# Kernel tuning notes

Measured on AMD Instinct MI355X. Metric: run time of the kernel, lower is better.

The kernel has to match this reference:

```python
import jax, jax.numpy as jnp
import numpy as np

B, TQ, TK, D, NA = 8, 512, 2048, 1024, 512
H, HD = 16, 64          # n_head, head_dim (D = H*HD)
NE, HID = 4, 32         # n_experts, expert hidden_dim
EPS = 1e-6


def _rmsnorm(x, w):
    return x * jax.lax.rsqrt(jnp.mean(x * x, axis=-1, keepdims=True) + EPS) * w


def setup_inputs() -> dict:
    key = jax.random.key(0)
    ks = jax.random.split(key, 20)
    r = lambda i, shp: jax.random.normal(ks[i], shp, dtype=jnp.float32) * 0.02
    return {
        'q': jax.random.normal(ks[0], (B, TQ, D), dtype=jnp.float32),
        'kv': jax.random.normal(ks[1], (B, TK, D), dtype=jnp.float32),
        'qn_w': jnp.ones((D,), jnp.float32),
        'kva_w': jnp.ones((D,), jnp.float32),
        'kvi_w': jnp.ones((D,), jnp.float32),
        'dn_w': jnp.ones((D,), jnp.float32),
        'fn_w': jnp.ones((D,), jnp.float32),
        'Wq': r(2, (D, D)), 'bq': jnp.zeros((D,), jnp.float32),
        'Wk': r(3, (D, D)), 'bk': jnp.zeros((D,), jnp.float32),
        'Wv': r(4, (D, D)), 'bv': jnp.zeros((D,), jnp.float32),
        'Wo': r(5, (D, D)), 'bo': jnp.zeros((D,), jnp.float32),
        'active_bias': r(6, (D,)),
        'inactive_bias': r(7, (D,)),
        'log_temp': jnp.array(0.0, jnp.float32),
        'gate_attn': jnp.array(0.3, jnp.float32),
        'gate_ffn': jnp.array(0.7, jnp.float32),
        'Wr': r(8, (D, NE)), 'br': jnp.zeros((NE,), jnp.float32),
        'W1': r(9, (NE, D, 2 * HID)), 'b1': jnp.zeros((NE, 2 * HID), jnp.float32),
        'W2': r(10, (NE, HID, D)), 'b2': jnp.zeros((NE, D), jnp.float32),
        'kv_mask': jnp.ones((B, TK), bool),
        'n_actives': NA,
    }


def _forward(q, kv, qn_w, kva_w, kvi_w, dn_w, fn_w,
             Wq, bq, Wk, bk, Wv, bv, Wo, bo,
             active_bias, inactive_bias, log_temp, gate_attn, gate_ffn,
             Wr, br, W1, b1, W2, b2, kv_mask, n_actives):
    Na = int(n_actives)
    Tk = kv.shape[1]
    Ni = Tk - Na
    b, tq, d = q.shape

    # split-normed kv, with active/inactive learned biases injected pre-KV-proj
    kv_a = _rmsnorm(kv[:, :Na], kva_w) + active_bias
    kv_i = _rmsnorm(kv[:, Na:], kvi_w) + inactive_bias
    kv_b = jnp.concatenate([kv_a, kv_i], axis=1)

    qn = _rmsnorm(q, qn_w)
    qp = (qn @ Wq + bq).reshape(b, tq, H, HD).transpose(0, 2, 1, 3)  # (B,H,Tq,hd)
    k = (kv_b @ Wk + bk).reshape(b, Tk, H, HD).transpose(0, 2, 1, 3)
    v = (kv_b @ Wv + bv).reshape(b, Tk, H, HD).transpose(0, 2, 1, 3)

    # torch: q *= 1/sqrt(hd), then SDPA(q/temp, ...) applies another 1/sqrt(hd)
    temp = jnp.clip(jnp.exp(log_temp), 0.1, 10.0)
    scale = 1.0 / (HD * temp)

    def attn(kk, vv):
        logits = jnp.einsum('bhqd,bhkd->bhqk', qp, kk) * scale
        return jnp.einsum('bhqk,bhkd->bhqd', jax.nn.softmax(logits, axis=-1), vv)

    out = attn(k[:, :, :Na], v[:, :, :Na]) / np.sqrt(max(Na, 1)) \
        - attn(k[:, :, Na:], v[:, :, Na:]) / np.sqrt(max(Ni, 1))
    out = out.transpose(0, 2, 1, 3).reshape(b, tq, d)
    delta = _rmsnorm(out @ Wo + bo, dn_w)
    q_new = q + jax.nn.sigmoid(gate_attn) * delta

    # dense soft MoE over normed kv, with query-similarity logit bias
    x = _rmsnorm(kv, fn_w)
    logits = x @ Wr + br                                   # (B,Tk,NE)
    q_vec = jnp.mean(q_new, axis=1, keepdims=True)         # (B,1,D)
    sim = jnp.einsum('bqd,btd->bt', q_vec, x)              # (B,Tk)
    probs = jax.nn.softmax(logits + sim[..., None], axis=-1)

    h = jnp.einsum('btd,edh->bteh', x, W1) + b1            # (B,Tk,NE,2*HID)
    xp, g = h[..., :HID], h[..., HID:]
    act = xp * (g * jax.nn.sigmoid(g))                     # SwiGLU
    eo = jnp.einsum('bteh,ehd->bted', act, W2) + b2        # (B,Tk,NE,D)
    moe_out = jnp.einsum('bte,bted->btd', probs, eo)

    kv_new = kv + jax.nn.sigmoid(gate_ffn) * moe_out
    return q_new, kv_new


def reference(q, kv, qn_w, kva_w, kvi_w, dn_w, fn_w,
              Wq, bq, Wk, bk, Wv, bv, Wo, bo,
              active_bias, inactive_bias, log_temp, gate_attn, gate_ffn,
              Wr, br, W1, b1, W2, b2, kv_mask, n_actives):
    return _forward(q, kv, qn_w, kva_w, kvi_w, dn_w, fn_w,
                    Wq, bq, Wk, bk, Wv, bv, Wo, bo,
                    active_bias, inactive_bias, log_temp, gate_attn, gate_ffn,
                    Wr, br, W1, b1, W2, b2, kv_mask, n_actives)
```

## Files before the change

### kernel.cpp

```cpp
#include <hip/hip_runtime.h>
#include <hip/hip_bf16.h>
#include <stdint.h>


#define B_   8
#define TQ_  512
#define TK_  2048
#define D_   1024
#define H_   16
#define HD_  64
#define NE_  4
#define HID_ 32
#define EPSF 1e-6f
#define LOG2E 1.44269504f

typedef __bf16 bf16_t;
typedef __bf16 bf16x8 __attribute__((ext_vector_type(8)));
typedef __bf16 bf16x4 __attribute__((ext_vector_type(4)));
typedef float  f32x4  __attribute__((ext_vector_type(4)));

typedef __attribute__((address_space(1))) void gvoid_t;
typedef __attribute__((address_space(3))) void lvoid_t;

__device__ __forceinline__ void gld_lds16(const void* g, void* l) {
  __builtin_amdgcn_global_load_lds((gvoid_t*)g, (lvoid_t*)l, 16, 0, 0);
}

struct TP4 { const float* in[4]; bf16_t* out[4]; };

__global__ void transpose_conv4_kernel(TP4 p) {
  __shared__ float tile[32][33];
  const int bz = blockIdx.z;
  const float* in = p.in[bz];
  bf16_t* out = p.out[bz];
  const int rb = blockIdx.y * 32, cb = blockIdx.x * 32;
  const int txi = threadIdx.x, tyi = threadIdx.y;
#pragma unroll
  for (int i = 0; i < 32; i += 8)
    tile[tyi + i][txi] = in[(size_t)(rb + tyi + i) * D_ + cb + txi];
  __syncthreads();
#pragma unroll
  for (int i = 0; i < 32; i += 8)
    out[(size_t)(cb + tyi + i) * D_ + rb + txi] = (bf16_t)tile[txi][tyi + i];
}

__global__ void transpose_conv_kernel(const float* __restrict__ in, bf16_t* __restrict__ out,
                                      int R, int C, int in_bstride,
                                      int out_rstride, int ob_row, int ob_col) {
  __shared__ float tile[32][33];
  const int bz = blockIdx.z;
  const int rb = blockIdx.y * 32, cb = blockIdx.x * 32;
  const int txi = threadIdx.x, tyi = threadIdx.y;
  const float* inp = in + (size_t)bz * in_bstride;
#pragma unroll
  for (int i = 0; i < 32; i += 8) {
    const int r = rb + tyi + i, c = cb + txi;
    if (r < R && c < C) tile[tyi + i][txi] = inp[(size_t)r * C + c];
  }
  __syncthreads();
#pragma unroll
  for (int i = 0; i < 32; i += 8) {
    const int orow = cb + tyi + i;
    const int ocol = rb + txi;
    if (orow < C && ocol < R)
      out[(size_t)(orow + bz * ob_row) * out_rstride + bz * ob_col + ocol] =
          (bf16_t)tile[txi][tyi + i];
  }
}

__device__ __forceinline__ float block_rsum(float v, float* red) {
  v += __shfl_xor(v, 1);  v += __shfl_xor(v, 2);  v += __shfl_xor(v, 4);
  v += __shfl_xor(v, 8);  v += __shfl_xor(v, 16); v += __shfl_xor(v, 32);
  const int tid = threadIdx.x;
  if ((tid & 63) == 0) red[tid >> 6] = v;
  __syncthreads();
  return red[0] + red[1] + red[2] + red[3];
}

__global__ __launch_bounds__(256)
void rms_kv_kernel(const float* __restrict__ kv, const float* __restrict__ kva_w,
                   const float* __restrict__ kvi_w, const float* __restrict__ fn_w,
                   const float* __restrict__ ab, const float* __restrict__ ib,
                   const int* __restrict__ n_act, const float* __restrict__ Wr,
                   const float* __restrict__ br,
                   bf16_t* __restrict__ kvb, bf16_t* __restrict__ xn,
                   float* __restrict__ probs) {
  __shared__ float red[4];
  __shared__ f32x4 pred[4];
  const int row = blockIdx.x;
  const int t = row & (TK_ - 1);
  const int tid = threadIdx.x;
  const float* src = kv + (size_t)row * D_;
  f32x4 v = ((const f32x4*)src)[tid];
  float ss = v[0]*v[0] + v[1]*v[1] + v[2]*v[2] + v[3]*v[3];
  ss = block_rsum(ss, red);
  const float rs = rsqrtf(ss * (1.0f / D_) + EPSF);
  const int Na = n_act[0];
  const float* wsel = (t < Na) ? kva_w : kvi_w;
  const float* bsel = (t < Na) ? ab : ib;
  const int d = tid * 4;
  f32x4 wv = *(const f32x4*)(wsel + d);
  f32x4 bv = *(const f32x4*)(bsel + d);
  f32x4 fv = *(const f32x4*)(fn_w + d);
  bf16x4 o0, o1;
  f32x4 p4 = {};
#pragma unroll
  for (int c = 0; c < 4; ++c) {
    const float xv = v[c] * rs;
    const float xf = xv * fv[c];
    o0[c] = (bf16_t)(xv * wv[c] + bv[c]);
    o1[c] = (bf16_t)xf;
    const f32x4 w4 = *(const f32x4*)&Wr[(d + c) * 4];
    p4 += w4 * xf;
  }
  *(bf16x4*)&kvb[(size_t)row * D_ + d] = o0;
  *(bf16x4*)&xn [(size_t)row * D_ + d] = o1;
#pragma unroll
  for (int m = 1; m <= 32; m <<= 1) {
    p4[0] += __shfl_xor(p4[0], m); p4[1] += __shfl_xor(p4[1], m);
    p4[2] += __shfl_xor(p4[2], m); p4[3] += __shfl_xor(p4[3], m);
  }
  if ((tid & 63) == 0) pred[tid >> 6] = p4;
  __syncthreads();
  if (tid == 0) {
    f32x4 s = pred[0] + pred[1] + pred[2] + pred[3];
    s[0] += br[0]; s[1] += br[1]; s[2] += br[2]; s[3] += br[3];
    const float mx = fmaxf(fmaxf(s[0], s[1]), fmaxf(s[2], s[3]));
    const float e0 = __expf(s[0] - mx), e1 = __expf(s[1] - mx);
    const float e2 = __expf(s[2] - mx), e3 = __expf(s[3] - mx);
    const float inv = 1.0f / (e0 + e1 + e2 + e3);
    f32x4 pr = { e0 * inv, e1 * inv, e2 * inv, e3 * inv };
    *(f32x4*)&probs[row * 4] = pr;
  }
}

__global__ __launch_bounds__(256)
void rms_q_kernel(const float* __restrict__ q, const float* __restrict__ qn_w,
                  bf16_t* __restrict__ qn) {
  __shared__ float red[4];
  const int row = blockIdx.x;
  const int tid = threadIdx.x;
  const float* src = q + (size_t)row * D_;
  f32x4 v = ((const f32x4*)src)[tid];
  float ss = v[0]*v[0] + v[1]*v[1] + v[2]*v[2] + v[3]*v[3];
  ss = block_rsum(ss, red);
  const float rs = rsqrtf(ss * (1.0f / D_) + EPSF);
  const int d = tid * 4;
  f32x4 wv = *(const f32x4*)(qn_w + d);
  bf16x4 o0;
#pragma unroll
  for (int c = 0; c < 4; ++c) o0[c] = (bf16_t)(v[c] * rs * wv[c]);
  *(bf16x4*)&qn[(size_t)row * D_ + d] = o0;
}

__device__ __forceinline__ int xcd_swz(int bx, int gx) {
  if ((gx & 7) == 0) { const int cpx = gx >> 3; return (bx & 7) * cpx + (bx >> 3); }
  return bx;
}

__global__ __launch_bounds__(256)
void gemm_kv(const bf16_t* __restrict__ A, const bf16_t* __restrict__ Wk,
             const bf16_t* __restrict__ Wv, const float* __restrict__ bk,
             const float* __restrict__ bv, bf16_t* __restrict__ Kout,
             bf16_t* __restrict__ Vt) {
  __shared__ alignas(16) bf16_t lds[3 * 8192];
  bf16_t* As  = lds;
  bf16_t* Bks = lds + 8192;
  bf16_t* Bvs = lds + 16384;
  const int K = D_;
  const int tid = threadIdx.x;
  const int lane = tid & 63;
  const int w = tid >> 6;
  const int wr = w >> 1, wc = w & 1;
  const int lane15 = lane & 15, lgrp = lane >> 4;

  const int flat = blockIdx.x;
  const int xcd = flat & 7;
  const int local = flat >> 3;
  const int tg = local >> 3;
  const int yy = local & 7;
  const int m0 = (xcd * 16 + tg) * 128;
  const int n0 = yy * 128;

  f32x4 acc_k[4][4] = {};
  f32x4 acc_v[4][4] = {};

  const bf16_t* ga = A  + (size_t)(m0 + (tid >> 2)) * K + (tid & 3) * 8;
  const bf16_t* gk = Wk + (size_t)(n0 + (tid >> 2)) * K + (tid & 3) * 8;
  const bf16_t* gv = Wv + (size_t)(n0 + (tid >> 2)) * K + (tid & 3) * 8;
  const size_t rstep = (size_t)64 * K;
  const int kb = lgrp * 8;
  const int ar  = ((wr * 64 + lane15) << 5) + kb;
  const int br2 = ((wc * 64 + lane15) << 5) + kb;

  gld_lds16(ga,         &As[tid * 8]);
  gld_lds16(ga + rstep, &As[2048 + tid * 8]);
  gld_lds16(gk,         &Bks[tid * 8]);
  gld_lds16(gk + rstep, &Bks[2048 + tid * 8]);
  gld_lds16(gv,         &Bvs[tid * 8]);
  gld_lds16(gv + rstep, &Bvs[2048 + tid * 8]);
  int buf = 0;
  for (int k0 = 0; k0 < K; k0 += 32) {
    __syncthreads();
    if (k0 + 32 < K) {
      const int nb = buf ^ 1;
      gld_lds16(ga + k0 + 32,         &As[nb * 4096 + tid * 8]);
      gld_lds16(ga + k0 + 32 + rstep, &As[nb * 4096 + 2048 + tid * 8]);
      gld_lds16(gk + k0 + 32,         &Bks[nb * 4096 + tid * 8]);
      gld_lds16(gk + k0 + 32 + rstep, &Bks[nb * 4096 + 2048 + tid * 8]);
      gld_lds16(gv + k0 + 32,         &Bvs[nb * 4096 + tid * 8]);
      gld_lds16(gv + k0 + 32 + rstep, &Bvs[nb * 4096 + 2048 + tid * 8]);
    }
    bf16x8 af[4], bkf[4], bvf[4];
#pragma unroll
    for (int i = 0; i < 4; ++i) af[i]  = *(const bf16x8*)&As [buf * 4096 + ar  + i * 512];
#pragma unroll
    for (int j = 0; j < 4; ++j) bkf[j] = *(const bf16x8*)&Bks[buf * 4096 + br2 + j * 512];
#pragma unroll
    for (int j = 0; j < 4; ++j) bvf[j] = *(const bf16x8*)&Bvs[buf * 4096 + br2 + j * 512];
    __builtin_amdgcn_s_setprio(1);
#pragma unroll
    for (int i = 0; i < 4; ++i)
#pragma unroll
      for (int j = 0; j < 4; ++j) {
        acc_k[i][j] = __builtin_amdgcn_mfma_f32_16x16x32_bf16(af[i], bkf[j], acc_k[i][j], 0, 0, 0);
        acc_v[i][j] = __builtin_amdgcn_mfma_f32_16x16x32_bf16(af[i], bvf[j], acc_v[i][j], 0, 0, 0);
      }
    __builtin_amdgcn_s_setprio(0);
    buf ^= 1;
  }

  const int row0 = m0 + wr * 64 + (lgrp << 2);
  const int col0 = n0 + wc * 64 + lane15;
#pragma unroll
  for (int j = 0; j < 4; ++j) {
    const int cc = col0 + j * 16;
    const float bkv = bk[cc];
#pragma unroll
    for (int i = 0; i < 4; ++i) {
      const int rr = row0 + i * 16;
#pragma unroll
      for (int r = 0; r < 4; ++r)
        Kout[(size_t)(rr + r) * D_ + cc] = (bf16_t)(acc_k[i][j][r] + bkv);
    }
  }

  __syncthreads();
  bf16_t* vt_l = lds + w * 4608;
#pragma unroll
  for (int j = 0; j < 4; ++j) {
    const int nl = j * 16 + lane15;
    const float bvv = bv[n0 + wc * 64 + nl];
#pragma unroll
    for (int i = 0; i < 4; ++i) {
      bf16x4 pv;
#pragma unroll
      for (int r = 0; r < 4; ++r) pv[r] = (bf16_t)(acc_v[i][j][r] + bvv);
      *(bf16x4*)&vt_l[nl * 72 + i * 16 + lgrp * 4] = pv;
    }
  }
  const int bidx2 = m0 >> 11;
  const int tok0 = (m0 & (TK_ - 1)) + wr * 64;
  bf16_t* vbase = Vt + (size_t)bidx2 * D_ * TK_ + (size_t)(n0 + wc * 64) * TK_ + tok0;
#pragma unroll
  for (int it = 0; it < 8; ++it) {
    const int ln = (lane >> 3) + it * 8;
    const int tk = (lane & 7) * 8;
    const bf16x8 v8 = *(const bf16x8*)&vt_l[ln * 72 + tk];
    *(bf16x8*)&vbase[(size_t)ln * TK_ + tk] = v8;
  }
}

__device__ __forceinline__ void gemm_loop_db(const bf16_t* __restrict__ ga,
                                             const bf16_t* __restrict__ gb,
                                             bf16_t* As, bf16_t* Bs, int K,
                                             size_t rstep, int ar, int br2,
                                             int tid, f32x4 acc[4][4]) {
  gld_lds16(ga,         &As[tid * 8]);
  gld_lds16(ga + rstep, &As[2048 + tid * 8]);
  gld_lds16(gb,         &Bs[tid * 8]);
  gld_lds16(gb + rstep, &Bs[2048 + tid * 8]);
  int buf = 0;
  for (int k0 = 0; k0 < K; k0 += 32) {
    __syncthreads();
    if (k0 + 32 < K) {
      const int nb = buf ^ 1;
      gld_lds16(ga + k0 + 32,         &As[nb * 4096 + tid * 8]);
      gld_lds16(ga + k0 + 32 + rstep, &As[nb * 4096 + 2048 + tid * 8]);
      gld_lds16(gb + k0 + 32,         &Bs[nb * 4096 + tid * 8]);
      gld_lds16(gb + k0 + 32 + rstep, &Bs[nb * 4096 + 2048 + tid * 8]);
    }
    bf16x8 af[4], bfr[4];
#pragma unroll
    for (int i = 0; i < 4; ++i) af[i]  = *(const bf16x8*)&As[buf * 4096 + ar  + i * 512];
#pragma unroll
    for (int j = 0; j < 4; ++j) bfr[j] = *(const bf16x8*)&Bs[buf * 4096 + br2 + j * 512];
#pragma unroll
    for (int i = 0; i < 4; ++i)
#pragma unroll
      for (int j = 0; j < 4; ++j)
        acc[i][j] = __builtin_amdgcn_mfma_f32_16x16x32_bf16(af[i], bfr[j], acc[i][j], 0, 0, 0);
    buf ^= 1;
  }
}

__device__ __forceinline__ void gemm64_loop_db(const bf16_t* __restrict__ ga,
                                               const bf16_t* __restrict__ gb,
                                               bf16_t* As, bf16_t* Bs, int K,
                                               size_t rstep, int ar, int br2,
                                               int tid, f32x4 acc[2][4]) {
  gld_lds16(ga,         &As[tid * 8]);
  gld_lds16(gb,         &Bs[tid * 8]);
  gld_lds16(gb + rstep, &Bs[2048 + tid * 8]);
  int buf = 0;
  for (int k0 = 0; k0 < K; k0 += 32) {
    __syncthreads();
    if (k0 + 32 < K) {
      const int nb = buf ^ 1;
      gld_lds16(ga + k0 + 32,         &As[nb * 2048 + tid * 8]);
      gld_lds16(gb + k0 + 32,         &Bs[nb * 4096 + tid * 8]);
      gld_lds16(gb + k0 + 32 + rstep, &Bs[nb * 4096 + 2048 + tid * 8]);
    }
    bf16x8 af[2], bfr[4];
#pragma unroll
    for (int i = 0; i < 2; ++i) af[i]  = *(const bf16x8*)&As[buf * 2048 + ar  + i * 512];
#pragma unroll
    for (int j = 0; j < 4; ++j) bfr[j] = *(const bf16x8*)&Bs[buf * 4096 + br2 + j * 512];
#pragma unroll
    for (int i = 0; i < 2; ++i)
#pragma unroll
      for (int j = 0; j < 4; ++j)
        acc[i][j] = __builtin_amdgcn_mfma_f32_16x16x32_bf16(af[i], bfr[j], acc[i][j], 0, 0, 0);
    buf ^= 1;
  }
}

template<int HAS_BIAS>
__global__ __launch_bounds__(256)
void gemm64_tn(const bf16_t* __restrict__ A, const bf16_t* __restrict__ Wt,
               const float* __restrict__ bias, bf16_t* __restrict__ C,
               int M, int N, int K) {
  __shared__ alignas(16) bf16_t As[2 * 64 * 32];
  __shared__ alignas(16) bf16_t Bs[2 * 128 * 32];
  const int tid = threadIdx.x;
  const int lane = tid & 63;
  const int w = tid >> 6;
  const int wr = w >> 1, wc = w & 1;
  const int m0 = xcd_swz(blockIdx.x, gridDim.x) * 64;
  const int n0 = blockIdx.y * 128;

  f32x4 acc[2][4] = {};
  const bf16_t* ga = A  + (size_t)(m0 + (tid >> 2)) * K + (tid & 3) * 8;
  const bf16_t* gb = Wt + (size_t)(n0 + (tid >> 2)) * K + (tid & 3) * 8;
  const int kb = (lane >> 4) * 8;
  const int ar  = ((wr * 32 + (lane & 15)) << 5) + kb;
  const int br2 = ((wc * 64 + (lane & 15)) << 5) + kb;

  gemm64_loop_db(ga, gb, As, Bs, K, (size_t)64 * K, ar, br2, tid, acc);

  const int row0 = m0 + wr * 32 + ((lane >> 4) << 2);
  const int col0 = n0 + wc * 64 + (lane & 15);
#pragma unroll
  for (int j = 0; j < 4; ++j) {
    const int cc = col0 + j * 16;
    const float bv = HAS_BIAS ? bias[cc] : 0.0f;
#pragma unroll
    for (int i = 0; i < 2; ++i) {
      const int rr = row0 + i * 16;
#pragma unroll
      for (int r = 0; r < 4; ++r)
        C[(size_t)(rr + r) * N + cc] = (bf16_t)(acc[i][j][r] + bv);
    }
  }
}

__global__ __launch_bounds__(256)
void gemm64_h_act(const bf16_t* __restrict__ A, const bf16_t* __restrict__ Wt,
                  const float* __restrict__ bias, const float* __restrict__ probs,
                  bf16_t* __restrict__ a2) {
  __shared__ alignas(16) bf16_t As[2 * 64 * 32];
  __shared__ alignas(16) bf16_t Bs[2 * 128 * 32];
  const int K = D_;
  const int tid = threadIdx.x;
  const int lane = tid & 63;
  const int w = tid >> 6;
  const int wr = w >> 1, wc = w & 1;
  const int m0 = xcd_swz(blockIdx.x, gridDim.x) * 64;
  const int n0 = blockIdx.y * 128;

  f32x4 acc[2][4] = {};
  const bf16_t* ga = A  + (size_t)(m0 + (tid >> 2)) * K + (tid & 3) * 8;
  const bf16_t* gb = Wt + (size_t)(n0 + (tid >> 2)) * K + (tid & 3) * 8;
  const int kb = (lane >> 4) * 8;
  const int ar  = ((wr * 32 + (lane & 15)) << 5) + kb;
  const int br2 = ((wc * 64 + (lane & 15)) << 5) + kb;

  gemm64_loop_db(ga, gb, As, Bs, K, (size_t)64 * K, ar, br2, tid, acc);

  const int row0 = m0 + wr * 32 + ((lane >> 4) << 2);
  const int hbase = n0 + wc * 64 + (lane & 15);
  const int e = hbase >> 6;
#pragma unroll
  for (int j = 0; j < 2; ++j) {
    const int ch = hbase + j * 16;
    const float bx = bias[ch], bg = bias[ch + 32];
    const int ac = (ch & 63) + e * 32;
#pragma unroll
    for (int i = 0; i < 2; ++i) {
      const int rr = row0 + i * 16;
#pragma unroll
      for (int r = 0; r < 4; ++r) {
        const float xp = acc[i][j][r] + bx;
        const float g  = acc[i][j + 2][r] + bg;
        const float sg = 1.0f / (1.0f + __expf(-g));
        const float pr = probs[(size_t)(rr + r) * 4 + e];
        a2[(size_t)(rr + r) * 128 + ac] = (bf16_t)(pr * xp * g * sg);
      }
    }
  }
}

__global__ __launch_bounds__(256)
void gemm_moe_kvnew(const bf16_t* __restrict__ A, const bf16_t* __restrict__ Wt,
                    const float* __restrict__ kv, const float* __restrict__ probs,
                    const float* __restrict__ b2, const float* __restrict__ gate_ffn,
                    float* __restrict__ out) {
  __shared__ alignas(16) bf16_t As[2 * 128 * 32];
  __shared__ alignas(16) bf16_t Bs[2 * 128 * 32];
  const int K = 128, N = D_;
  const int tid = threadIdx.x;
  const int lane = tid & 63;
  const int w = tid >> 6;
  const int wr = w >> 1, wc = w & 1;
  const int m0 = xcd_swz(blockIdx.x, gridDim.x) * 128;
  const int n0 = blockIdx.y * 128;

  f32x4 acc[4][4] = {};
  const bf16_t* ga = A  + (size_t)(m0 + (tid >> 2)) * K + (tid & 3) * 8;
  const bf16_t* gb = Wt + (size_t)(n0 + (tid >> 2)) * K + (tid & 3) * 8;
  const int kb = (lane >> 4) * 8;
  const int ar  = ((wr * 64 + (lane & 15)) << 5) + kb;
  const int br2 = ((wc * 64 + (lane & 15)) << 5) + kb;

  gemm_loop_db(ga, gb, As, Bs, K, (size_t)64 * K, ar, br2, tid, acc);

  const float sgf = 1.0f / (1.0f + __expf(-gate_ffn[0]));
  const int row0 = m0 + wr * 64 + ((lane >> 4) << 2);
  const int col0 = n0 + wc * 64 + (lane & 15);
#pragma unroll
  for (int j = 0; j < 4; ++j) {
    const int cc = col0 + j * 16;
    const f32x4 b2v = { b2[0 * D_ + cc], b2[1 * D_ + cc], b2[2 * D_ + cc], b2[3 * D_ + cc] };
#pragma unroll
    for (int i = 0; i < 4; ++i) {
      const int rr = row0 + i * 16;
#pragma unroll
      for (int r = 0; r < 4; ++r) {
        const f32x4 pr = *(const f32x4*)&probs[(size_t)(rr + r) * 4];
        const float bsum = pr[0]*b2v[0] + pr[1]*b2v[1] + pr[2]*b2v[2] + pr[3]*b2v[3];
        out[(size_t)(rr + r) * N + cc] =
            kv[(size_t)(rr + r) * N + cc] + sgf * (acc[i][j][r] + bsum);
      }
    }
  }
}

__global__ __launch_bounds__(128, 2)
void attn_mfma_kernel(const bf16_t* __restrict__ qp, const bf16_t* __restrict__ kb,
                      const bf16_t* __restrict__ vt, bf16_t* __restrict__ attno,
                      const float* __restrict__ log_temp, const int* __restrict__ n_act) {
  __shared__ alignas(16) bf16_t Ks[2][64 * 64];
  __shared__ alignas(16) bf16_t Vs[2][64 * 64];
  __shared__ alignas(16) bf16_t Ps[2][32 * 64];

  const int dd = blockIdx.x;
  const int xcd = dd & 7, within = dd >> 3;
  const int qt = within & 7, slot0 = within >> 3;
  const int bh = slot0 * 8 + xcd;
  const int b = bh >> 4, h = bh & 15;

  const int tid = threadIdx.x;
  const int lane = tid & 63;
  const int w = tid >> 6;
  const int lane15 = lane & 15, lgrp = lane >> 4, l7 = lane & 7;
  const int Na = n_act[0];
  float temp = __expf(log_temp[0]);
  temp = fminf(fmaxf(temp, 0.1f), 10.0f);
  const float lsc = LOG2E / (64.0f * temp);
  const int rowbase = qt * 64 + w * 32;

  const bf16_t* qsrcA = qp + (size_t)(b * TQ_ + rowbase + lane15) * D_ + h * 64 + lgrp * 8;
  const bf16_t* qsrcB = qsrcA + (size_t)16 * D_;
  bf16x8 qfA0 = *(const bf16x8*)qsrcA;
  bf16x8 qfA1 = *(const bf16x8*)(qsrcA + 32);
  bf16x8 qfB0 = *(const bf16x8*)qsrcB;
  bf16x8 qfB1 = *(const bf16x8*)(qsrcB + 32);
#pragma unroll
  for (int j = 0; j < 8; ++j) {
    qfA0[j] = (bf16_t)((float)qfA0[j] * lsc);
    qfA1[j] = (bf16_t)((float)qfA1[j] * lsc);
    qfB0[j] = (bf16_t)((float)qfB0[j] * lsc);
    qfB1[j] = (bf16_t)((float)qfB1[j] * lsc);
  }

  const int srow = tid >> 3;
  const int schunk = (tid & 7) ^ (srow & 7);
  const bf16_t* ksrc = kb + (size_t)(b * TK_ + srow) * D_ + h * 64 + schunk * 8;
  const bf16_t* vsrc = vt + ((size_t)(b * 16 + h) * 64 + srow) * TK_ + schunk * 8;

  f32x4 oA[4] = {}, oB[4] = {}, outA[4] = {}, outB[4] = {};
  float laccA = 0.f, laccB = 0.f;

  const float inv_sa = rsqrtf((float)(Na > 1 ? Na : 1));
  const int Ni = TK_ - Na;
  const float inv_si = rsqrtf((float)(Ni > 1 ? Ni : 1));

#pragma unroll
  for (int r = 0; r < 4; ++r) {
    gld_lds16(ksrc + (size_t)r * 16 * D_, &Ks[0][r * 1024 + tid * 8]);
    gld_lds16(vsrc + (size_t)r * 16 * TK_, &Vs[0][r * 1024 + tid * 8]);
  }

  for (int t = 0; t < TK_ / 64; ++t) {
    const int cur = t & 1;
    __syncthreads();
    if (t + 1 < TK_ / 64) {
      const int nb = cur ^ 1;
      const bf16_t* kN = ksrc + (size_t)(t + 1) * 64 * D_;
      const bf16_t* vN = vsrc + (size_t)(t + 1) * 64;
#pragma unroll
      for (int r = 0; r < 4; ++r) {
        gld_lds16(kN + (size_t)r * 16 * D_, &Ks[nb][r * 1024 + tid * 8]);
        gld_lds16(vN + (size_t)r * 16 * TK_, &Vs[nb][r * 1024 + tid * 8]);
      }
    }

    f32x4 sA[4], sB[4];
    __builtin_amdgcn_s_setprio(1);
#pragma unroll
    for (int cf = 0; cf < 4; ++cf) {
      const int krow = (cf * 16 + lane15) * 64;
      const bf16x8 kf0 = *(const bf16x8*)&Ks[cur][krow + ((lgrp ^ l7) << 3)];
      const bf16x8 kf1 = *(const bf16x8*)&Ks[cur][krow + (((lgrp + 4) ^ l7) << 3)];
      f32x4 s = {};
      s = __builtin_amdgcn_mfma_f32_16x16x32_bf16(kf0, qfA0, s, 0, 0, 0);
      s = __builtin_amdgcn_mfma_f32_16x16x32_bf16(kf1, qfA1, s, 0, 0, 0);
      sA[cf] = s;
      f32x4 s2 = {};
      s2 = __builtin_amdgcn_mfma_f32_16x16x32_bf16(kf0, qfB0, s2, 0, 0, 0);
      s2 = __builtin_amdgcn_mfma_f32_16x16x32_bf16(kf1, qfB1, s2, 0, 0, 0);
      sB[cf] = s2;
    }
    __builtin_amdgcn_s_setprio(0);

#pragma unroll
    for (int cf = 0; cf < 4; ++cf) {
      const int c = cf * 2 + (lgrp >> 1);
      const int pcol = ((c ^ l7) << 3) + (lgrp & 1) * 4;
      f32x4 pA, pB;
#pragma unroll
      for (int r = 0; r < 4; ++r) pA[r] = exp2f(sA[cf][r]);
#pragma unroll
      for (int r = 0; r < 4; ++r) pB[r] = exp2f(sB[cf][r]);
      laccA += (pA[0] + pA[1]) + (pA[2] + pA[3]);
      laccB += (pB[0] + pB[1]) + (pB[2] + pB[3]);
      bf16x4 pvA, pvB;
#pragma unroll
      for (int r = 0; r < 4; ++r) { pvA[r] = (bf16_t)pA[r]; pvB[r] = (bf16_t)pB[r]; }
      *(bf16x4*)&Ps[w][lane15 * 64 + pcol]        = pvA;
      *(bf16x4*)&Ps[w][(16 + lane15) * 64 + pcol] = pvB;
    }

    {
      const int prowA = lane15 * 64;
      const int prowB = (16 + lane15) * 64;
      const bf16x8 paA0 = *(const bf16x8*)&Ps[w][prowA + ((lgrp ^ l7) << 3)];
      const bf16x8 paA1 = *(const bf16x8*)&Ps[w][prowA + (((lgrp + 4) ^ l7) << 3)];
      const bf16x8 paB0 = *(const bf16x8*)&Ps[w][prowB + ((lgrp ^ l7) << 3)];
      const bf16x8 paB1 = *(const bf16x8*)&Ps[w][prowB + (((lgrp + 4) ^ l7) << 3)];
      __builtin_amdgcn_s_setprio(1);
#pragma unroll
      for (int df = 0; df < 4; ++df) {
        const int vrow = (df * 16 + lane15) * 64;
        const bf16x8 vf0 = *(const bf16x8*)&Vs[cur][vrow + ((lgrp ^ l7) << 3)];
        const bf16x8 vf1 = *(const bf16x8*)&Vs[cur][vrow + (((lgrp + 4) ^ l7) << 3)];
        oA[df] = __builtin_amdgcn_mfma_f32_16x16x32_bf16(paA0, vf0, oA[df], 0, 0, 0);
        oA[df] = __builtin_amdgcn_mfma_f32_16x16x32_bf16(paA1, vf1, oA[df], 0, 0, 0);
        oB[df] = __builtin_amdgcn_mfma_f32_16x16x32_bf16(paB0, vf0, oB[df], 0, 0, 0);
        oB[df] = __builtin_amdgcn_mfma_f32_16x16x32_bf16(paB1, vf1, oB[df], 0, 0, 0);
      }
      __builtin_amdgcn_s_setprio(0);
    }

    const bool endA = ((t + 1) * 64 == Na);
    const bool endI = (t == TK_ / 64 - 1);
    if (endA || endI) {
      float lA = laccA, lB = laccB;
      lA += __shfl_xor(lA, 16); lA += __shfl_xor(lA, 32);
      lB += __shfl_xor(lB, 16); lB += __shfl_xor(lB, 32);
      const float ssc = endA ? inv_sa : -inv_si;
      f32x4 ivA, ivB;
#pragma unroll
      for (int r = 0; r < 4; ++r) {
        ivA[r] = ssc / __shfl(lA, lgrp * 4 + r);
        ivB[r] = ssc / __shfl(lB, lgrp * 4 + r);
      }
#pragma unroll
      for (int df = 0; df < 4; ++df) {
        outA[df] += oA[df] * ivA; oA[df] = (f32x4){};
        outB[df] += oB[df] * ivB; oB[df] = (f32x4){};
      }
      laccA = 0.f; laccB = 0.f;
    }
  }

#pragma unroll
  for (int df = 0; df < 4; ++df)
#pragma unroll
    for (int r = 0; r < 4; ++r) {
      const size_t ro = (size_t)(b * TQ_ + rowbase + lgrp * 4 + r) * D_ + h * 64 + df * 16 + lane15;
      attno[ro]           = (bf16_t)outA[df][r];
      attno[ro + 16 * D_] = (bf16_t)outB[df][r];
    }
}

__global__ __launch_bounds__(256)
void delta_qnew_kernel(const bf16_t* __restrict__ proj, const float* __restrict__ dn_w,
                       const float* __restrict__ q, const float* __restrict__ gate_attn,
                       float* __restrict__ qnew) {
  __shared__ float red[4];
  const int row = blockIdx.x;
  const int tid = threadIdx.x;
  bf16x4 pv = *(const bf16x4*)(proj + (size_t)row * D_ + tid * 4);
  f32x4 v;
#pragma unroll
  for (int c = 0; c < 4; ++c) v[c] = (float)pv[c];
  float ss = v[0]*v[0] + v[1]*v[1] + v[2]*v[2] + v[3]*v[3];
  ss = block_rsum(ss, red);
  const float rs = rsqrtf(ss * (1.0f / D_) + EPSF);
  const float sga = 1.0f / (1.0f + __expf(-gate_attn[0]));
  const int d = tid * 4;
  f32x4 wv = *(const f32x4*)(dn_w + d);
  f32x4 qv = *(const f32x4*)(q + (size_t)row * D_ + d);
  f32x4 out;
#pragma unroll
  for (int c = 0; c < 4; ++c) out[c] = qv[c] + sga * (v[c] * rs * wv[c]);
  *(f32x4*)&qnew[(size_t)row * D_ + d] = out;
}

extern "C" void kernel_launch(void* const* d_in, const int* in_sizes, int n_in,
                              void* d_out, int out_size, void* d_ws, size_t ws_size,
                              hipStream_t stream) {
  const float* q           = (const float*)d_in[0];
  const float* kv          = (const float*)d_in[1];
  const float* qn_w        = (const float*)d_in[2];
  const float* kva_w       = (const float*)d_in[3];
  const float* kvi_w       = (const float*)d_in[4];
  const float* dn_w        = (const float*)d_in[5];
  const float* fn_w        = (const float*)d_in[6];
  const float* Wq          = (const float*)d_in[7];
  const float* bq          = (const float*)d_in[8];
  const float* Wk          = (const float*)d_in[9];
  const float* bk          = (const float*)d_in[10];
  const float* Wv          = (const float*)d_in[11];
  const float* bv          = (const float*)d_in[12];
  const float* Wo          = (const float*)d_in[13];
  const float* bo          = (const float*)d_in[14];
  const float* active_bias = (const float*)d_in[15];
  const float* inactive_b  = (const float*)d_in[16];
  const float* log_temp    = (const float*)d_in[17];
  const float* gate_attn   = (const float*)d_in[18];
  const float* gate_ffn    = (const float*)d_in[19];
  const float* Wr          = (const float*)d_in[20];
  const float* br          = (const float*)d_in[21];
  const float* W1          = (const float*)d_in[22];
  const float* b1          = (const float*)d_in[23];
  const float* W2          = (const float*)d_in[24];
  const float* b2          = (const float*)d_in[25];
  const int*   n_act       = (const int*)d_in[27];

  char* ws = (char*)d_ws;
  size_t off = 0;
  auto alloc = [&](size_t bytes) -> char* {
    char* p = ws + off;
    off = (off + bytes + 255) & ~(size_t)255;
    return p;
  };

  bf16_t* wqT  = (bf16_t*)alloc((size_t)D_ * D_ * 2);
  bf16_t* wkT  = (bf16_t*)alloc((size_t)D_ * D_ * 2);
  bf16_t* wvT  = (bf16_t*)alloc((size_t)D_ * D_ * 2);
  bf16_t* woT  = (bf16_t*)alloc((size_t)D_ * D_ * 2);
  bf16_t* w1T  = (bf16_t*)alloc((size_t)256 * D_ * 2);
  bf16_t* w2T  = (bf16_t*)alloc((size_t)D_ * 128 * 2);
  bf16_t* kvb  = (bf16_t*)alloc((size_t)B_ * TK_ * D_ * 2);
  bf16_t* xn   = (bf16_t*)alloc((size_t)B_ * TK_ * D_ * 2);
  bf16_t* qn   = (bf16_t*)alloc((size_t)B_ * TQ_ * D_ * 2);
  bf16_t* qp   = (bf16_t*)alloc((size_t)B_ * TQ_ * D_ * 2);
  bf16_t* kbuf = (bf16_t*)alloc((size_t)B_ * TK_ * D_ * 2);
  bf16_t* vt   = (bf16_t*)alloc((size_t)B_ * D_ * TK_ * 2);
  float*  probs = (float*)alloc((size_t)B_ * TK_ * NE_ * 4);
  bf16_t* attno = qn;
  bf16_t* proj  = qp;
  bf16_t* a2buf = kbuf;
  (void)ws_size; (void)in_sizes; (void)n_in; (void)out_size;

  float* q_new_out  = (float*)d_out;
  float* kv_new_out = (float*)d_out + (size_t)B_ * TQ_ * D_;

  dim3 tb(32, 8);
  TP4 tp;
  tp.in[0] = Wq; tp.in[1] = Wk; tp.in[2] = Wv; tp.in[3] = Wo;
  tp.out[0] = wqT; tp.out[1] = wkT; tp.out[2] = wvT; tp.out[3] = woT;
  transpose_conv4_kernel<<<dim3(32, 32, 4), tb, 0, stream>>>(tp);
  transpose_conv_kernel<<<dim3(2, 32, 4), tb, 0, stream>>>(W1, w1T, D_, 64, D_ * 64, D_, 64, 0);
  transpose_conv_kernel<<<dim3(32, 1, 4), tb, 0, stream>>>(W2, w2T, 32, D_, 32 * D_, 128, 0, 32);

  rms_kv_kernel<<<B_ * TK_, 256, 0, stream>>>(kv, kva_w, kvi_w, fn_w, active_bias,
                                              inactive_b, n_act, Wr, br, kvb, xn, probs);
  rms_q_kernel<<<B_ * TQ_, 256, 0, stream>>>(q, qn_w, qn);

  gemm64_tn<1><<<dim3(B_ * TQ_ / 64, D_ / 128), 256, 0, stream>>>(qn, wqT, bq, qp, B_ * TQ_, D_, D_);
  gemm_kv<<<B_ * TK_ / 128 * (D_ / 128), 256, 0, stream>>>(kvb, wkT, wvT, bk, bv, kbuf, vt);

  attn_mfma_kernel<<<B_ * H_ * (TQ_ / 64), 128, 0, stream>>>(qp, kbuf, vt, attno, log_temp, n_act);

  gemm64_tn<1><<<dim3(B_ * TQ_ / 64, D_ / 128), 256, 0, stream>>>(attno, woT, bo, proj, B_ * TQ_, D_, D_);
  delta_qnew_kernel<<<B_ * TQ_, 256, 0, stream>>>(proj, dn_w, q, gate_attn, q_new_out);

  gemm64_h_act<<<dim3(B_ * TK_ / 64, 2), 256, 0, stream>>>(xn, w1T, b1, probs, a2buf);
  gemm_moe_kvnew<<<dim3(B_ * TK_ / 128, D_ / 128), 256, 0, stream>>>(a2buf, w2T, kv, probs, b2,
                                                                     gate_ffn, kv_new_out);
}
```

Measured before the change: 339.8 us.

## Triple-buffer KV projection GEMM with swizzled LDS layout and explicit vmcnt waits

Moves the fused K/V projection GEMM from double to triple buffering in LDS. Tiles are prefetched two steps ahead, and each step waits with an explicit s_waitcnt vmcnt plus a raw barrier instead of __syncthreads, so global loads overlap more with MFMA work. An XOR swizzle of the 8-element k-chunk is applied to the global source address and to the LDS read offsets, aimed at reducing LDS bank conflicts. LDS use grows from 48KB to 72KB per block, which may lower occupancy, and correctness depends on the exact vmcnt count matching the six loads issued per stage.

```diff
diff --git a/kernel.cpp b/kernel.cpp
--- a/kernel.cpp
+++ b/kernel.cpp
@@ -163,10 +163,10 @@
              const bf16_t* __restrict__ Wv, const float* __restrict__ bk,
              const float* __restrict__ bv, bf16_t* __restrict__ Kout,
              bf16_t* __restrict__ Vt) {
-  __shared__ alignas(16) bf16_t lds[3 * 8192];
+  __shared__ alignas(16) bf16_t lds[9 * 4096];
   bf16_t* As  = lds;
-  bf16_t* Bks = lds + 8192;
-  bf16_t* Bvs = lds + 16384;
+  bf16_t* Bks = lds + 3 * 4096;
+  bf16_t* Bvs = lds + 6 * 4096;
   const int K = D_;
   const int tid = threadIdx.x;
   const int lane = tid & 63;
@@ -185,39 +185,47 @@
   f32x4 acc_k[4][4] = {};
   f32x4 acc_v[4][4] = {};
 
-  const bf16_t* ga = A  + (size_t)(m0 + (tid >> 2)) * K + (tid & 3) * 8;
-  const bf16_t* gk = Wk + (size_t)(n0 + (tid >> 2)) * K + (tid & 3) * 8;
-  const bf16_t* gv = Wv + (size_t)(n0 + (tid >> 2)) * K + (tid & 3) * 8;
+  const int srow = tid >> 2;
+  const int swzs = ((srow ^ (srow >> 2)) & 3) << 3;
+  const int schunk = (((tid & 3) << 3) ^ swzs);
+  const bf16_t* ga = A  + (size_t)(m0 + srow) * K + schunk;
+  const bf16_t* gk = Wk + (size_t)(n0 + srow) * K + schunk;
+  const bf16_t* gv = Wv + (size_t)(n0 + srow) * K + schunk;
   const size_t rstep = (size_t)64 * K;
-  const int kb = lgrp * 8;
-  const int ar  = ((wr * 64 + lane15) << 5) + kb;
-  const int br2 = ((wc * 64 + lane15) << 5) + kb;
-
-  gld_lds16(ga,         &As[tid * 8]);
-  gld_lds16(ga + rstep, &As[2048 + tid * 8]);
-  gld_lds16(gk,         &Bks[tid * 8]);
-  gld_lds16(gk + rstep, &Bks[2048 + tid * 8]);
-  gld_lds16(gv,         &Bvs[tid * 8]);
-  gld_lds16(gv + rstep, &Bvs[2048 + tid * 8]);
-  int buf = 0;
-  for (int k0 = 0; k0 < K; k0 += 32) {
-    __syncthreads();
-    if (k0 + 32 < K) {
-      const int nb = buf ^ 1;
-      gld_lds16(ga + k0 + 32,         &As[nb * 4096 + tid * 8]);
-      gld_lds16(ga + k0 + 32 + rstep, &As[nb * 4096 + 2048 + tid * 8]);
-      gld_lds16(gk + k0 + 32,         &Bks[nb * 4096 + tid * 8]);
-      gld_lds16(gk + k0 + 32 + rstep, &Bks[nb * 4096 + 2048 + tid * 8]);
-      gld_lds16(gv + k0 + 32,         &Bvs[nb * 4096 + tid * 8]);
-      gld_lds16(gv + k0 + 32 + rstep, &Bvs[nb * 4096 + 2048 + tid * 8]);
-    }
+
+  const int swzr = ((lane15 ^ (lane15 >> 2)) & 3) << 3;
+  const int kbs  = (lgrp << 3) ^ swzr;
+  const int ar   = ((wr * 64 + lane15) << 5) + kbs;
+  const int br2  = ((wc * 64 + lane15) << 5) + kbs;
+
+  auto STAGE = [&](int t, int bufi) {
+    const int off = bufi * 4096;
+    const int k0 = t * 32;
+    gld_lds16(ga + k0,         &As [off + tid * 8]);
+    gld_lds16(ga + k0 + rstep, &As [off + 2048 + tid * 8]);
+    gld_lds16(gk + k0,         &Bks[off + tid * 8]);
+    gld_lds16(gk + k0 + rstep, &Bks[off + 2048 + tid * 8]);
+    gld_lds16(gv + k0,         &Bvs[off + tid * 8]);
+    gld_lds16(gv + k0 + rstep, &Bvs[off + 2048 + tid * 8]);
+  };
+
+  STAGE(0, 0);
+  STAGE(1, 1);
+
+  const int NSTEP = K / 32;
+  for (int t = 0; t < NSTEP; ++t) {
+    if (t < NSTEP - 1) asm volatile("s_waitcnt vmcnt(6)" ::: "memory");
+    else               asm volatile("s_waitcnt vmcnt(0)" ::: "memory");
+    __builtin_amdgcn_s_barrier();
+    if (t + 2 < NSTEP) STAGE(t + 2, (t + 2) % 3);
+    const int off = (t % 3) * 4096;
     bf16x8 af[4], bkf[4], bvf[4];
 #pragma unroll
-    for (int i = 0; i < 4; ++i) af[i]  = *(const bf16x8*)&As [buf * 4096 + ar  + i * 512];
-#pragma unroll
-    for (int j = 0; j < 4; ++j) bkf[j] = *(const bf16x8*)&Bks[buf * 4096 + br2 + j * 512];
-#pragma unroll
-    for (int j = 0; j < 4; ++j) bvf[j] = *(const bf16x8*)&Bvs[buf * 4096 + br2 + j * 512];
+    for (int i = 0; i < 4; ++i) af[i]  = *(const bf16x8*)&As [off + ar  + i * 512];
+#pragma unroll
+    for (int j = 0; j < 4; ++j) bkf[j] = *(const bf16x8*)&Bks[off + br2 + j * 512];
+#pragma unroll
+    for (int j = 0; j < 4; ++j) bvf[j] = *(const bf16x8*)&Bvs[off + br2 + j * 512];
     __builtin_amdgcn_s_setprio(1);
 #pragma unroll
     for (int i = 0; i < 4; ++i)
@@ -227,7 +235,6 @@
         acc_v[i][j] = __builtin_amdgcn_mfma_f32_16x16x32_bf16(af[i], bvf[j], acc_v[i][j], 0, 0, 0);
       }
     __builtin_amdgcn_s_setprio(0);
-    buf ^= 1;
   }
 
   const int row0 = m0 + wr * 64 + (lgrp << 2);
```

Measured after the change: 366.6 us. 7.9% more time.

## Pre-pack KV GEMM operands in MFMA fragment order for contiguous LDS staging

Applied to the files above, without the earlier changes.

The normalized kv activations and the Wk/Wv weights are now written in a tiled layout that matches the MFMA fragment order (128-row tiles, 32-wide k-slices, lane-major). The K/V GEMM can then stage each k-slice with fully contiguous 16-byte global-to-LDS copies and read fragments with simple lane-strided offsets. This targets strided global reads and the LDS access pattern in the largest GEMM. In exchange, the producer kernels do more scattered 8-byte writes, and Wk/Wv need their own transpose kernel.

```diff
diff --git a/kernel.cpp b/kernel.cpp
--- a/kernel.cpp
+++ b/kernel.cpp
@@ -26,9 +26,9 @@
   __builtin_amdgcn_global_load_lds((gvoid_t*)g, (lvoid_t*)l, 16, 0, 0);
 }
 
-struct TP4 { const float* in[4]; bf16_t* out[4]; };
-
-__global__ void transpose_conv4_kernel(TP4 p) {
+struct TP2 { const float* in[2]; bf16_t* out[2]; };
+
+__global__ void transpose_conv2_kernel(TP2 p) {
   __shared__ float tile[32][33];
   const int bz = blockIdx.z;
   const float* in = p.in[bz];
@@ -42,6 +42,32 @@
 #pragma unroll
   for (int i = 0; i < 32; i += 8)
     out[(size_t)(cb + tyi + i) * D_ + rb + txi] = (bf16_t)tile[txi][tyi + i];
+}
+
+__global__ void transpose_fragorder_kernel(TP2 p) {
+  __shared__ float tile[32][33];
+  const float* in = p.in[blockIdx.z];
+  bf16_t* out = p.out[blockIdx.z];
+  const int kb0 = blockIdx.y * 32;
+  const int nb0 = blockIdx.x * 32;
+  const int tx = threadIdx.x, ty = threadIdx.y;
+#pragma unroll
+  for (int i = 0; i < 32; i += 8)
+    tile[ty + i][tx] = in[(size_t)(kb0 + ty + i) * D_ + nb0 + tx];
+  __syncthreads();
+  const int t = ty * 32 + tx;
+  const int n_l = t >> 3;
+  const int k_l = (t & 7) * 4;
+  const int n = nb0 + n_l;
+  const int k = kb0 + k_l;
+  const int tile_n = n >> 7, rn = n & 127, hc = rn >> 6, rr = rn & 63;
+  const int j = rr >> 4, l15 = rr & 15;
+  const int s = k >> 5, lg = (k >> 3) & 3, e = k & 7;
+  bf16x4 o;
+#pragma unroll
+  for (int c = 0; c < 4; ++c) o[c] = (bf16_t)tile[k_l + c][n_l];
+  *(bf16x4*)&out[(size_t)tile_n * 131072 + s * 4096 + hc * 2048 +
+                 j * 512 + (lg * 16 + l15) * 8 + e] = o;
 }
 
 __global__ void transpose_conv_kernel(const float* __restrict__ in, bf16_t* __restrict__ out,
@@ -113,8 +139,14 @@
     const f32x4 w4 = *(const f32x4*)&Wr[(d + c) * 4];
     p4 += w4 * xf;
   }
-  *(bf16x4*)&kvb[(size_t)row * D_ + d] = o0;
-  *(bf16x4*)&xn [(size_t)row * D_ + d] = o1;
+  {
+    const int rl = row & 127, hh = rl >> 6, rr2 = rl & 63;
+    const int ii = rr2 >> 4, l15 = rr2 & 15;
+    const int s2 = d >> 5, lg2 = (d >> 3) & 3, e2 = d & 7;
+    *(bf16x4*)&kvb[(size_t)(row >> 7) * 131072 + s2 * 4096 + hh * 2048 +
+                   ii * 512 + (lg2 * 16 + l15) * 8 + e2] = o0;
+  }
+  *(bf16x4*)&xn[(size_t)row * D_ + d] = o1;
 #pragma unroll
   for (int m = 1; m <= 32; m <<= 1) {
     p4[0] += __shfl_xor(p4[0], m); p4[1] += __shfl_xor(p4[1], m);
@@ -167,7 +199,6 @@
   bf16_t* As  = lds;
   bf16_t* Bks = lds + 8192;
   bf16_t* Bvs = lds + 16384;
-  const int K = D_;
   const int tid = threadIdx.x;
   const int lane = tid & 63;
   const int w = tid >> 6;
@@ -185,39 +216,36 @@
   f32x4 acc_k[4][4] = {};
   f32x4 acc_v[4][4] = {};
 
-  const bf16_t* ga = A  + (size_t)(m0 + (tid >> 2)) * K + (tid & 3) * 8;
-  const bf16_t* gk = Wk + (size_t)(n0 + (tid >> 2)) * K + (tid & 3) * 8;
-  const bf16_t* gv = Wv + (size_t)(n0 + (tid >> 2)) * K + (tid & 3) * 8;
-  const size_t rstep = (size_t)64 * K;
-  const int kb = lgrp * 8;
-  const int ar  = ((wr * 64 + lane15) << 5) + kb;
-  const int br2 = ((wc * 64 + lane15) << 5) + kb;
-
-  gld_lds16(ga,         &As[tid * 8]);
-  gld_lds16(ga + rstep, &As[2048 + tid * 8]);
-  gld_lds16(gk,         &Bks[tid * 8]);
-  gld_lds16(gk + rstep, &Bks[2048 + tid * 8]);
-  gld_lds16(gv,         &Bvs[tid * 8]);
-  gld_lds16(gv + rstep, &Bvs[2048 + tid * 8]);
+  const bf16_t* ga = A  + (size_t)(m0 >> 7) * 131072 + tid * 8;
+  const bf16_t* gk = Wk + (size_t)(n0 >> 7) * 131072 + tid * 8;
+  const bf16_t* gv = Wv + (size_t)(n0 >> 7) * 131072 + tid * 8;
+
+  auto STAGE = [&](int s, int bufi) {
+    const int off = bufi * 4096;
+    const size_t so = (size_t)s * 4096;
+    gld_lds16(ga + so,        &As [off + tid * 8]);
+    gld_lds16(ga + so + 2048, &As [off + 2048 + tid * 8]);
+    gld_lds16(gk + so,        &Bks[off + tid * 8]);
+    gld_lds16(gk + so + 2048, &Bks[off + 2048 + tid * 8]);
+    gld_lds16(gv + so,        &Bvs[off + tid * 8]);
+    gld_lds16(gv + so + 2048, &Bvs[off + 2048 + tid * 8]);
+  };
+
+  STAGE(0, 0);
   int buf = 0;
-  for (int k0 = 0; k0 < K; k0 += 32) {
+  const int abase0 = wr * 2048 + lane * 8;
+  const int bbase0 = wc * 2048 + lane * 8;
+  for (int s = 0; s < 32; ++s) {
     __syncthreads();
-    if (k0 + 32 < K) {
-      const int nb = buf ^ 1;
-      gld_lds16(ga + k0 + 32,         &As[nb * 4096 + tid * 8]);
-      gld_lds16(ga + k0 + 32 + rstep, &As[nb * 4096 + 2048 + tid * 8]);
-      gld_lds16(gk + k0 + 32,         &Bks[nb * 4096 + tid * 8]);
-      gld_lds16(gk + k0 + 32 + rstep, &Bks[nb * 4096 + 2048 + tid * 8]);
-      gld_lds16(gv + k0 + 32,         &Bvs[nb * 4096 + tid * 8]);
-      gld_lds16(gv + k0 + 32 + rstep, &Bvs[nb * 4096 + 2048 + tid * 8]);
-    }
+    if (s + 1 < 32) STAGE(s + 1, buf ^ 1);
+    const int off = buf * 4096;
     bf16x8 af[4], bkf[4], bvf[4];
 #pragma unroll
-    for (int i = 0; i < 4; ++i) af[i]  = *(const bf16x8*)&As [buf * 4096 + ar  + i * 512];
-#pragma unroll
-    for (int j = 0; j < 4; ++j) bkf[j] = *(const bf16x8*)&Bks[buf * 4096 + br2 + j * 512];
-#pragma unroll
-    for (int j = 0; j < 4; ++j) bvf[j] = *(const bf16x8*)&Bvs[buf * 4096 + br2 + j * 512];
+    for (int i = 0; i < 4; ++i) af[i]  = *(const bf16x8*)&As [off + abase0 + i * 512];
+#pragma unroll
+    for (int j = 0; j < 4; ++j) bkf[j] = *(const bf16x8*)&Bks[off + bbase0 + j * 512];
+#pragma unroll
+    for (int j = 0; j < 4; ++j) bvf[j] = *(const bf16x8*)&Bvs[off + bbase0 + j * 512];
     __builtin_amdgcn_s_setprio(1);
 #pragma unroll
     for (int i = 0; i < 4; ++i)
@@ -709,10 +737,10 @@
   float* kv_new_out = (float*)d_out + (size_t)B_ * TQ_ * D_;
 
   dim3 tb(32, 8);
-  TP4 tp;
-  tp.in[0] = Wq; tp.in[1] = Wk; tp.in[2] = Wv; tp.in[3] = Wo;
-  tp.out[0] = wqT; tp.out[1] = wkT; tp.out[2] = wvT; tp.out[3] = woT;
-  transpose_conv4_kernel<<<dim3(32, 32, 4), tb, 0, stream>>>(tp);
+  TP2 tpa; tpa.in[0] = Wq; tpa.in[1] = Wo; tpa.out[0] = wqT; tpa.out[1] = woT;
+  transpose_conv2_kernel<<<dim3(32, 32, 2), tb, 0, stream>>>(tpa);
+  TP2 tpf; tpf.in[0] = Wk; tpf.in[1] = Wv; tpf.out[0] = wkT; tpf.out[1] = wvT;
+  transpose_fragorder_kernel<<<dim3(32, 32, 2), tb, 0, stream>>>(tpf);
   transpose_conv_kernel<<<dim3(2, 32, 4), tb, 0, stream>>>(W1, w1T, D_, 64, D_ * 64, D_, 64, 0);
   transpose_conv_kernel<<<dim3(32, 1, 4), tb, 0, stream>>>(W2, w2T, 32, D_, 32 * D_, 128, 0, 32);
 
```

Measured after the change: 352.0 us. 3.6% more time.
